# Performance work log

Hardware: AMD Instinct MI355X
Metric: run time of the kernel (lower is better)

## Reference

```python
import jax, jax.numpy as jnp
import numpy as np

D = 64        # inner_feature_len (dim)
HID = 128     # hidden_channels of the edge MLP
NCONV = 2     # n_conv
STEPS = 3     # Set2Set processing_steps
NSEG = 128    # number of graphs in the batch


def setup_inputs() -> dict:
    key = jax.random.key(0)
    ks = jax.random.split(key, 30)
    N, E, FN, FE = 10000, 64000, 92, 41
    s = 0.05
    p = lambda i, shape: jax.random.normal(ks[i], shape, jnp.float32) * s
    return {
        "x": jax.random.normal(ks[0], (N, FN), jnp.float32),
        "edge_attr": jax.random.uniform(ks[1], (E, FE), dtype=jnp.float32),
        "lin0_w": p(2, (D, FN)), "lin0_b": p(3, (D,)),
        "nn1_w": p(4, (HID, FE)), "nn1_b": p(5, (HID,)),
        "nn2_w": p(6, (D * D, HID)), "nn2_b": p(7, (D * D,)),
        "root_w": p(8, (D, D)), "conv_b": p(9, (D,)),
        "gru_w_ih": p(10, (3 * D, D)), "gru_w_hh": p(11, (3 * D, D)),
        "gru_b_ih": p(12, (3 * D,)), "gru_b_hh": p(13, (3 * D,)),
        "lstm_w_ih": p(14, (4 * D, 2 * D)), "lstm_w_hh": p(15, (4 * D, D)),
        "lstm_b_ih": p(16, (4 * D,)), "lstm_b_hh": p(17, (4 * D,)),
        "lin1_w": p(18, (D, 2 * D)), "lin1_b": p(19, (D,)),
        "lin2_w": p(20, (1, D)), "lin2_b": p(21, (1,)),
        "edge_index": jax.random.randint(ks[22], (2, E), 0, N, dtype=jnp.int32),
        "batch": jnp.sort(jax.random.randint(ks[23], (N,), 0, NSEG, dtype=jnp.int32)),
    }


def _gru_step(m, h, w_ih, w_hh, b_ih, b_hh):
    # torch GRU gate order: r, z, n
    gi = m @ w_ih.T + b_ih
    gh = h @ w_hh.T + b_hh
    r = jax.nn.sigmoid(gi[:, :D] + gh[:, :D])
    z = jax.nn.sigmoid(gi[:, D:2 * D] + gh[:, D:2 * D])
    n = jnp.tanh(gi[:, 2 * D:] + r * gh[:, 2 * D:])
    return (1.0 - z) * n + z * h


def _forward(x, edge_attr, lin0_w, lin0_b, nn1_w, nn1_b, nn2_w, nn2_b, root_w, conv_b,
             gru_w_ih, gru_w_hh, gru_b_ih, gru_b_hh, lstm_w_ih, lstm_w_hh, lstm_b_ih,
             lstm_b_hh, lin1_w, lin1_b, lin2_w, lin2_b, edge_index, batch):
    N = x.shape[0]
    src, dst = edge_index[0], edge_index[1]

    # Edge-conditioned weight matrices: [E, D, D] (dominant intermediate)
    We = (jax.nn.relu(edge_attr @ nn1_w.T + nn1_b) @ nn2_w.T + nn2_b).reshape(-1, D, D)
    deg = jnp.clip(jax.ops.segment_sum(jnp.ones_like(src, jnp.float32), dst, num_segments=N), 1.0, None)

    out = jax.nn.relu(x @ lin0_w.T + lin0_b)   # [N, D]
    h = out                                     # GRU hidden (num_layers=1)
    for _ in range(NCONV):
        # NNConv: gather -> per-edge matmul -> scatter-mean, plus root transform + bias
        msg = jnp.einsum('ei,eio->eo', out[src], We)                 # [E, D]
        agg = jax.ops.segment_sum(msg, dst, num_segments=N) / deg[:, None]
        m = jax.nn.relu(agg + out @ root_w.T + conv_b)
        h = _gru_step(m, h, gru_w_ih, gru_w_hh, gru_b_ih, gru_b_hh)
        out = h

    # Set2Set pooling (LSTM-attention readout)
    q_star = jnp.zeros((NSEG, 2 * D), x.dtype)
    hl = jnp.zeros((NSEG, D), x.dtype)
    cl = jnp.zeros((NSEG, D), x.dtype)
    for _ in range(STEPS):
        g = q_star @ lstm_w_ih.T + lstm_b_ih + hl @ lstm_w_hh.T + lstm_b_hh
        i = jax.nn.sigmoid(g[:, :D])
        f = jax.nn.sigmoid(g[:, D:2 * D])
        gg = jnp.tanh(g[:, 2 * D:3 * D])
        o = jax.nn.sigmoid(g[:, 3 * D:])
        cl = f * cl + i * gg
        hl = o * jnp.tanh(cl)
        q = hl                                   # [NSEG, D]
        e = jnp.sum(out * q[batch], axis=-1)     # [N]
        mmax = jax.ops.segment_max(e, batch, num_segments=NSEG)
        a = jnp.exp(e - mmax[batch])
        denom = jax.ops.segment_sum(a, batch, num_segments=NSEG)
        a = a / denom[batch]
        r = jax.ops.segment_sum(a[:, None] * out, batch, num_segments=NSEG)  # [NSEG, D]
        q_star = jnp.concatenate([q, r], axis=1)

    y = jax.nn.relu(q_star @ lin1_w.T + lin1_b) @ lin2_w.T + lin2_b
    return y.reshape(-1)


def reference(x, edge_attr, lin0_w, lin0_b, nn1_w, nn1_b, nn2_w, nn2_b, root_w, conv_b,
              gru_w_ih, gru_w_hh, gru_b_ih, gru_b_hh, lstm_w_ih, lstm_w_hh, lstm_b_ih,
              lstm_b_hh, lin1_w, lin1_b, lin2_w, lin2_b, edge_index, batch):
    return _forward(x, edge_attr, lin0_w, lin0_b, nn1_w, nn1_b, nn2_w, nn2_b, root_w,
                    conv_b, gru_w_ih, gru_w_hh, gru_b_ih, gru_b_hh, lstm_w_ih, lstm_w_hh,
                    lstm_b_ih, lstm_b_hh, lin1_w, lin1_b, lin2_w, lin2_b, edge_index, batch)
```

## Files before the change

### kernel.cpp

```cpp
#include <hip/hip_runtime.h>
#include <hip/hip_bf16.h>
#include <math.h>

#define DD 64
#define HIDC 128
#define FN 92
#define FE 41
#define S2CAP 192

typedef unsigned short u16;
typedef short bf16x8 __attribute__((ext_vector_type(8)));
typedef float f32x4 __attribute__((ext_vector_type(4)));
typedef u16 u16x8 __attribute__((ext_vector_type(8)));

__device__ __forceinline__ float sigmoidf_(float x){ return 1.f/(1.f+expf(-x)); }

__device__ __forceinline__ u16 f2bf(float v){
  union { float f; unsigned u; } x; x.f = v;
  unsigned r = x.u + 0x7fff + ((x.u >> 16) & 1);
  return (u16)(r >> 16);
}
__device__ __forceinline__ float bf2f(u16 v){
  union { float f; unsigned u; } x; x.u = ((unsigned)v) << 16;
  return x.f;
}
__device__ __forceinline__ void split_bf(float v, u16& h, u16& l){
  h = f2bf(v); l = f2bf(v - bf2f(h));
}

__global__ void k_pack(const float* __restrict__ lin0_w, const float* __restrict__ nn1_w,
                       const float* __restrict__ root_w, const float* __restrict__ gwih,
                       const float* __restrict__ gwhh, const float* __restrict__ lwih,
                       const float* __restrict__ lwhh, const float* __restrict__ lin1_w,
                       float* __restrict__ lin0T, float* __restrict__ nn1T,
                       float* __restrict__ rootT, float* __restrict__ wihT,
                       float* __restrict__ whhT, float* __restrict__ lwihT,
                       float* __restrict__ lwhhT, float* __restrict__ lin1T)
{
  int idx = blockIdx.x*blockDim.x + threadIdx.x;
  if (idx < 92*64){ int k=idx/64, o=idx%64; lin0T[k*64+o] = lin0_w[o*92+k]; return; } idx -= 92*64;
  if (idx < 41*128){ int k=idx/128, h=idx%128; nn1T[k*128+h] = nn1_w[h*41+k]; return; } idx -= 41*128;
  if (idx < 64*64){ int i=idx/64, o=idx%64; rootT[i*64+o] = root_w[o*64+i]; return; } idx -= 64*64;
  if (idx < 64*192){ int i=idx/192, g=idx%192; wihT[i*192+g] = gwih[g*64+i]; return; } idx -= 64*192;
  if (idx < 64*192){ int i=idx/192, g=idx%192; whhT[i*192+g] = gwhh[g*64+i]; return; } idx -= 64*192;
  if (idx < 128*256){ int j=idx/256, t=idx%256; lwihT[j*256+t] = lwih[t*128+j]; return; } idx -= 128*256;
  if (idx < 64*256){ int j=idx/256, t=idx%256; lwhhT[j*256+t] = lwhh[t*64+j]; return; } idx -= 64*256;
  if (idx < 128*64){ int j=idx/64, t=idx%64; lin1T[j*64+t] = lin1_w[t*128+j]; return; }
}

__global__ void k_pack_b2(const float* __restrict__ nn2_w,
                          u16* __restrict__ BhT, u16* __restrict__ BlT){
  int idx = blockIdx.x*256 + threadIdx.x;
  if (idx >= 524288) return;
  int i  = idx & 63;
  int ho = (idx >> 6) & 4095;
  int c  = idx >> 18;
  int h = ho >> 6, o = ho & 63;
  float v = nn2_w[(size_t)(i*64+o)*128 + c*64 + h];
  u16 hi, lo; split_bf(v, hi, lo);
  BhT[idx] = hi; BlT[idx] = lo;
}

__global__ void k_pack_b1(const float* __restrict__ nn1_w,
                          u16* __restrict__ BT1h, u16* __restrict__ BT1l){
  int idx = blockIdx.x*256 + threadIdx.x;
  if (idx >= 8192) return;
  int h = idx >> 6, k = idx & 63;
  float v = (k < FE) ? nn1_w[(size_t)h*FE + k] : 0.f;
  u16 hi, lo; split_bf(v, hi, lo);
  BT1h[idx] = hi; BT1l[idx] = lo;
}

__global__ void k_split_ea(const float* __restrict__ ea, const int* __restrict__ sortedE,
                           u16* __restrict__ eaH, u16* __restrict__ eaL, int E){
  int idx = blockIdx.x*256 + threadIdx.x;
  if (idx >= E*64) return;
  int ew = idx >> 6, k = idx & 63;
  int e = sortedE[ew];
  float v = (k < FE) ? ea[(size_t)e*FE + k] : 0.f;
  u16 hi, lo; split_bf(v, hi, lo);
  eaH[idx] = hi; eaL[idx] = lo;
}

__global__ __launch_bounds__(256) void k_node_mlp(const float* __restrict__ x,
    const float* __restrict__ lin0T, const float* __restrict__ lin0_b,
    const float* __restrict__ nn2_b,
    float* __restrict__ out, u16* __restrict__ outH, u16* __restrict__ outL,
    float* __restrict__ bterm, int N)
{
  __shared__ float xs[16][FN];
  const int w = threadIdx.x>>6, o = threadIdx.x&63;
  const int nb = blockIdx.x*16 + w*4;
  for (int idx = o; idx < 4*FN; idx += 64){
    int j = idx/FN, k = idx%FN;
    int n = nb + j;
    xs[w*4+j][k] = (n<N) ? x[(size_t)n*FN + k] : 0.f;
  }
  float acc[4];
  float bv = lin0_b[o];
  #pragma unroll
  for (int j=0;j<4;j++) acc[j] = bv;
  for (int k=0;k<FN;k++){
    float lw = lin0T[k*64+o];
    #pragma unroll
    for (int j=0;j<4;j++) acc[j] = fmaf(xs[w*4+j][k], lw, acc[j]);
  }
  float v[4];
  #pragma unroll
  for (int j=0;j<4;j++){
    v[j] = fmaxf(acc[j], 0.f);
    int n = nb + j;
    if (n < N){
      out[(size_t)n*64+o] = v[j];
      u16 hi, lo; split_bf(v[j], hi, lo);
      outH[(size_t)n*64+o] = hi;
      outL[(size_t)n*64+o] = lo;
    }
  }
  float bt[4] = {0.f,0.f,0.f,0.f};
  for (int i=0;i<64;i++){
    float wnb = nn2_b[i*64+o];
    #pragma unroll
    for (int j=0;j<4;j++) bt[j] = fmaf(__shfl(v[j], i, 64), wnb, bt[j]);
  }
  #pragma unroll
  for (int j=0;j<4;j++){
    int n = nb + j;
    if (n < N) bterm[(size_t)n*64+o] = bt[j];
  }
}

__global__ void k_count(const int* __restrict__ dst, const int* __restrict__ src,
                        float* __restrict__ deg, int* __restrict__ scnt, int E){
  int e = blockIdx.x*blockDim.x + threadIdx.x;
  if (e < E){
    atomicAdd(&deg[dst[e]], 1.f);
    atomicAdd(&scnt[src[e]], 1);
  }
}

__global__ void k_scan1(const int* __restrict__ cnt, int* __restrict__ excl,
                        int* __restrict__ bsum, int N){
  __shared__ int buf[256];
  int i = blockIdx.x*256 + threadIdx.x;
  int v = (i<N) ? cnt[i] : 0;
  buf[threadIdx.x] = v;
  __syncthreads();
  #pragma unroll
  for (int off=1; off<256; off<<=1){
    int t = (threadIdx.x>=off) ? buf[threadIdx.x-off] : 0;
    __syncthreads();
    buf[threadIdx.x] += t;
    __syncthreads();
  }
  if (i<N) excl[i] = buf[threadIdx.x] - v;
  if (threadIdx.x==255) bsum[blockIdx.x] = buf[255];
}
__global__ void k_scan2(int* __restrict__ bsum, int nb){
  __shared__ int buf[256];
  int v = (threadIdx.x<nb) ? bsum[threadIdx.x] : 0;
  buf[threadIdx.x] = v;
  __syncthreads();
  #pragma unroll
  for (int off=1; off<256; off<<=1){
    int t = (threadIdx.x>=off) ? buf[threadIdx.x-off] : 0;
    __syncthreads();
    buf[threadIdx.x] += t;
    __syncthreads();
  }
  if (threadIdx.x<nb) bsum[threadIdx.x] = buf[threadIdx.x] - v;
}
__global__ void k_scan3(int* __restrict__ starts, int* __restrict__ cursor,
                        const int* __restrict__ bsum, int N, int E){
  int i = blockIdx.x*256 + threadIdx.x;
  if (i<N){
    int s = starts[i] + bsum[blockIdx.x];
    starts[i] = s;
    cursor[i] = s;
  }
  if (i==0) starts[N] = E;
}

__global__ void k_sort(const int* __restrict__ src, const int* __restrict__ dst,
                       int* __restrict__ cursor, int* __restrict__ sortedE,
                       int* __restrict__ dstS, int E){
  int e = blockIdx.x*256 + threadIdx.x;
  if (e < E){
    int s = src[e];
    int p = atomicAdd(&cursor[s], 1);
    sortedE[p] = e;
    dstS[p] = dst[e];
  }
}

__global__ __launch_bounds__(256,3) void k_edge_mlp_mfma(
    const u16* __restrict__ eaH, const u16* __restrict__ eaL,
    const u16* __restrict__ BT1h, const u16* __restrict__ BT1l,
    const float* __restrict__ nn1_b, float* __restrict__ hidden, int E)
{
  const int lane = threadIdx.x & 63;
  const int wave = threadIdx.x >> 6;
  const int row  = lane & 15;
  const int quad = lane >> 4;
  const int m0 = blockIdx.x*128 + (wave>>1)*64;
  const int n0 = (wave&1)*64;

  bf16x8 AH0[4], AH1[4], AL0[4], AL1[4];
  #pragma unroll
  for (int p=0;p<4;p++){
    int ar = min(m0 + p*16 + row, E-1);
    const u16* aH = eaH + (size_t)ar*64 + quad*8;
    const u16* aL = eaL + (size_t)ar*64 + quad*8;
    AH0[p] = *(const bf16x8*)(aH);
    AH1[p] = *(const bf16x8*)(aH + 32);
    AL0[p] = *(const bf16x8*)(aL);
    AL1[p] = *(const bf16x8*)(aL + 32);
  }
  #pragma unroll
  for (int tb=0;tb<4;tb++){
    const u16* bH = BT1h + (size_t)(n0 + tb*16 + row)*64 + quad*8;
    const u16* bL = BT1l + (size_t)(n0 + tb*16 + row)*64 + quad*8;
    bf16x8 bh0 = *(const bf16x8*)(bH);
    bf16x8 bh1 = *(const bf16x8*)(bH + 32);
    bf16x8 bl0 = *(const bf16x8*)(bL);
    bf16x8 bl1 = *(const bf16x8*)(bL + 32);
    float4 bias;
    {
      int nb = n0 + tb*16 + quad*4;
      bias.x = nn1_b[nb+0]; bias.y = nn1_b[nb+1];
      bias.z = nn1_b[nb+2]; bias.w = nn1_b[nb+3];
    }
    #pragma unroll
    for (int ta=0;ta<4;ta++){
      f32x4 a = {0.f,0.f,0.f,0.f};
      a = __builtin_amdgcn_mfma_f32_16x16x32_bf16(bh0, AH0[ta], a, 0,0,0);
      a = __builtin_amdgcn_mfma_f32_16x16x32_bf16(bh1, AH1[ta], a, 0,0,0);
      a = __builtin_amdgcn_mfma_f32_16x16x32_bf16(bl0, AH0[ta], a, 0,0,0);
      a = __builtin_amdgcn_mfma_f32_16x16x32_bf16(bl1, AH1[ta], a, 0,0,0);
      a = __builtin_amdgcn_mfma_f32_16x16x32_bf16(bh0, AL0[ta], a, 0,0,0);
      a = __builtin_amdgcn_mfma_f32_16x16x32_bf16(bh1, AL1[ta], a, 0,0,0);
      int m = m0 + ta*16 + row;
      if (m < E){
        float4 v;
        v.x = fmaxf(a[0]+bias.x, 0.f); v.y = fmaxf(a[1]+bias.y, 0.f);
        v.z = fmaxf(a[2]+bias.z, 0.f); v.w = fmaxf(a[3]+bias.w, 0.f);
        *(float4*)(hidden + (size_t)m*128 + n0 + tb*16 + quad*4) = v;
      }
    }
  }
}

__global__ __launch_bounds__(256,3) void k_qgemm_mfma(
    const u16* __restrict__ Ah, const u16* __restrict__ Al,
    const u16* __restrict__ BhT, const u16* __restrict__ BlT,
    u16* __restrict__ C, int M, int QS, int cbase)
{
  const int lane = threadIdx.x & 63;
  const int wave = threadIdx.x >> 6;
  const int row  = lane & 15;
  const int quad = lane >> 4;
  const int m0 = blockIdx.y * 64;
  const int col = cbase + blockIdx.x * 256 + wave * 64;
  const int chunk = col >> 12;
  const int n0 = col & 4095;
  const u16* Bh = BhT + (size_t)chunk*262144;
  const u16* Bl = BlT + (size_t)chunk*262144;

  bf16x8 AH0[4], AH1[4], AL0[4], AL1[4];
  #pragma unroll
  for (int p=0;p<4;p++){
    int ar = min(m0 + p*16 + row, M-1);
    const u16* aH = Ah + (size_t)ar*64 + quad*8;
    const u16* aL = Al + (size_t)ar*64 + quad*8;
    AH0[p] = *(const bf16x8*)(aH);
    AH1[p] = *(const bf16x8*)(aH + 32);
    AL0[p] = *(const bf16x8*)(aL);
    AL1[p] = *(const bf16x8*)(aL + 32);
  }

  f32x4 acc[4][4];
  #pragma unroll
  for (int ta=0;ta<4;ta++)
    #pragma unroll
    for (int tb=0;tb<4;tb++)
      acc[ta][tb] = (f32x4){0.f,0.f,0.f,0.f};

  #pragma unroll
  for (int tb=0;tb<4;tb++){
    const u16* bH = Bh + (size_t)(n0 + tb*16 + row)*64 + quad*8;
    const u16* bL = Bl + (size_t)(n0 + tb*16 + row)*64 + quad*8;
    bf16x8 bh0 = *(const bf16x8*)(bH);
    bf16x8 bh1 = *(const bf16x8*)(bH + 32);
    bf16x8 bl0 = *(const bf16x8*)(bL);
    bf16x8 bl1 = *(const bf16x8*)(bL + 32);
    #pragma unroll
    for (int ta=0;ta<4;ta++){
      f32x4 a = acc[ta][tb];
      a = __builtin_amdgcn_mfma_f32_16x16x32_bf16(bh0, AH0[ta], a, 0,0,0);
      a = __builtin_amdgcn_mfma_f32_16x16x32_bf16(bh1, AH1[ta], a, 0,0,0);
      a = __builtin_amdgcn_mfma_f32_16x16x32_bf16(bl0, AH0[ta], a, 0,0,0);
      a = __builtin_amdgcn_mfma_f32_16x16x32_bf16(bl1, AH1[ta], a, 0,0,0);
      a = __builtin_amdgcn_mfma_f32_16x16x32_bf16(bh0, AL0[ta], a, 0,0,0);
      a = __builtin_amdgcn_mfma_f32_16x16x32_bf16(bh1, AL1[ta], a, 0,0,0);
      acc[ta][tb] = a;
    }
  }

  #pragma unroll
  for (int ta=0;ta<4;ta++){
    int m = m0 + ta*16 + row;
    if (m >= M) continue;
    u16* dst = C + (size_t)m*QS + (col - cbase) + quad*8;
    #pragma unroll
    for (int p=0;p<2;p++){
      f32x4 aa = acc[ta][2*p];
      f32x4 ab = acc[ta][2*p+1];
      u16x8 v;
      v[0]=f2bf(aa[0]); v[1]=f2bf(aa[1]); v[2]=f2bf(aa[2]); v[3]=f2bf(aa[3]);
      v[4]=f2bf(ab[0]); v[5]=f2bf(ab[1]); v[6]=f2bf(ab[2]); v[7]=f2bf(ab[3]);
      *(u16x8*)(dst + p*32) = v;
    }
  }
}

template<int NH>
__global__ __launch_bounds__(256) void k_edge_gather(const u16* __restrict__ Q,
    const float* __restrict__ hidden, int h0, int addbt,
    const float* __restrict__ bterm, const int* __restrict__ starts,
    const int* __restrict__ dstS, float* __restrict__ agg, int N)
{
  constexpr int NJ = NH/4;
  constexpr int QS = NH*64;
  __shared__ float red[4][64];
  const int wv = threadIdx.x>>6, lane = threadIdx.x&63;
  const int n = blockIdx.x*4 + wv;
  if (n >= N) return;
  const int e0 = starts[n], e1 = starts[n+1];
  if (e0 >= e1) return;
  const int sg = lane>>4, oq = lane&15;
  const int posb = ((oq>>3)<<5) + ((oq&3)<<3) + (((oq>>2)&1)<<2);
  const u16* qp = Q + (size_t)n*QS + sg*64 + posb;
  ushort4 qreg[NJ];
  #pragma unroll
  for (int j=0;j<NJ;j++) qreg[j] = *(const ushort4*)(qp + (size_t)j*256);
  const float bt = addbt ? bterm[(size_t)n*64 + lane] : 0.f;

  float hA = hidden[(size_t)e0*128 + h0 + lane];
  float hB = (NH==128) ? hidden[(size_t)e0*128 + h0 + 64 + lane] : 0.f;
  int dN = dstS[e0];
  for (int e=e0; e<e1; ++e){
    const float h0v = hA, h1v = hB;
    const int d = dN;
    if (e+1 < e1){
      hA = hidden[(size_t)(e+1)*128 + h0 + lane];
      if (NH==128) hB = hidden[(size_t)(e+1)*128 + h0 + 64 + lane];
      dN = dstS[e+1];
    }
    float a0=0.f,a1=0.f,a2=0.f,a3=0.f;
    #pragma unroll
    for (int j=0;j<NJ;j++){
      float h4 = __shfl((j<16) ? h0v : h1v, ((j*4)&63)+sg, 64);
      a0 = fmaf(h4, bf2f(qreg[j].x), a0);
      a1 = fmaf(h4, bf2f(qreg[j].y), a1);
      a2 = fmaf(h4, bf2f(qreg[j].z), a2);
      a3 = fmaf(h4, bf2f(qreg[j].w), a3);
    }
    a0 += __shfl_xor(a0,16); a0 += __shfl_xor(a0,32);
    a1 += __shfl_xor(a1,16); a1 += __shfl_xor(a1,32);
    a2 += __shfl_xor(a2,16); a2 += __shfl_xor(a2,32);
    a3 += __shfl_xor(a3,16); a3 += __shfl_xor(a3,32);
    if (lane < 16){
      float4 r; r.x=a0; r.y=a1; r.z=a2; r.w=a3;
      *(float4*)&red[wv][lane*4] = r;
    }
    atomicAdd(&agg[(size_t)d*64 + lane], bt + red[wv][lane]);
  }
}

__global__ __launch_bounds__(256) void k_node_update(const float* __restrict__ outOld,
    const float* __restrict__ agg, const float* __restrict__ deg,
    const float* __restrict__ rootT, const float* __restrict__ conv_b,
    const float* __restrict__ wihT, const float* __restrict__ whhT,
    const float* __restrict__ b_ih, const float* __restrict__ b_hh,
    const float* __restrict__ nn2_b,
    float* __restrict__ outNew, u16* __restrict__ outH, u16* __restrict__ outL,
    float* __restrict__ bterm, int N)
{
  __shared__ float hs[16][64];
  __shared__ float ms[16][64];
  const int w = threadIdx.x>>6, o = threadIdx.x&63;
  const int nb = blockIdx.x*16 + w*4;
  float h[4];
  #pragma unroll
  for (int j=0;j<4;j++){
    int n = nb+j;
    h[j] = (n<N) ? outOld[(size_t)n*64+o] : 0.f;
    hs[w*4+j][o] = h[j];
  }
  float root[4] = {0.f,0.f,0.f,0.f};
  for (int i=0;i<64;i++){
    float rw = rootT[i*64+o];
    #pragma unroll
    for (int j=0;j<4;j++) root[j] = fmaf(hs[w*4+j][i], rw, root[j]);
  }
  float cb = conv_b[o];
  float m[4];
  #pragma unroll
  for (int j=0;j<4;j++){
    int n = nb+j;
    float d = (n<N) ? fmaxf(deg[n], 1.f) : 1.f;
    float a = (n<N) ? agg[(size_t)n*64+o]/d : 0.f;
    m[j] = fmaxf(a + root[j] + cb, 0.f);
    ms[w*4+j][o] = m[j];
  }
  float gir[4],giz[4],gin[4],ghr[4],ghz[4],ghn[4];
  float bir=b_ih[o], biz=b_ih[64+o], bin=b_ih[128+o];
  float bhr=b_hh[o], bhz=b_hh[64+o], bhn=b_hh[128+o];
  #pragma unroll
  for (int j=0;j<4;j++){
    gir[j]=bir; giz[j]=biz; gin[j]=bin;
    ghr[j]=bhr; ghz[j]=bhz; ghn[j]=bhn;
  }
  for (int i=0;i<64;i++){
    float wr=wihT[i*192+o], wz=wihT[i*192+64+o], wn=wihT[i*192+128+o];
    float vr=whhT[i*192+o], vz=whhT[i*192+64+o], vn=whhT[i*192+128+o];
    #pragma unroll
    for (int j=0;j<4;j++){
      float mi = ms[w*4+j][i], hi = hs[w*4+j][i];
      gir[j]=fmaf(mi,wr,gir[j]); giz[j]=fmaf(mi,wz,giz[j]); gin[j]=fmaf(mi,wn,gin[j]);
      ghr[j]=fmaf(hi,vr,ghr[j]); ghz[j]=fmaf(hi,vz,ghz[j]); ghn[j]=fmaf(hi,vn,ghn[j]);
    }
  }
  float v[4];
  #pragma unroll
  for (int j=0;j<4;j++){
    float r = sigmoidf_(gir[j]+ghr[j]);
    float z = sigmoidf_(giz[j]+ghz[j]);
    float nn = tanhf(gin[j] + r*ghn[j]);
    v[j] = (1.f-z)*nn + z*h[j];
    int n = nb+j;
    if (n<N){
      outNew[(size_t)n*64+o] = v[j];
      u16 hi16, lo16; split_bf(v[j], hi16, lo16);
      outH[(size_t)n*64+o] = hi16;
      outL[(size_t)n*64+o] = lo16;
    }
  }
  float bt[4] = {0.f,0.f,0.f,0.f};
  for (int i=0;i<64;i++){
    float wnb = nn2_b[i*64+o];
    #pragma unroll
    for (int j=0;j<4;j++) bt[j] = fmaf(__shfl(v[j], i, 64), wnb, bt[j]);
  }
  #pragma unroll
  for (int j=0;j<4;j++){
    int n = nb+j;
    if (n<N) bterm[(size_t)n*64+o] = bt[j];
  }
}

__global__ __launch_bounds__(256) void k_set2set(const float* __restrict__ out,
    const int* __restrict__ batch, int N,
    const float* __restrict__ lwihT, const float* __restrict__ lwhhT,
    const float* __restrict__ b_ih, const float* __restrict__ b_hh,
    const float* __restrict__ lin1T, const float* __restrict__ lin1_b,
    const float* __restrict__ lin2_w, const float* __restrict__ lin2_b,
    float* __restrict__ y)
{
  __shared__ float X[S2CAP][65];
  __shared__ float earr[S2CAP];
  __shared__ float qstar[128], hl[64], cl[64], g[256];
  __shared__ float rpart[4][64], spart[4], redm[4], zs[64];
  __shared__ int sb[2];
  const int tid = threadIdx.x;
  const int b = blockIdx.x;
  const int wid = tid>>6, lane = tid&63;
  if (tid < 128) qstar[tid] = 0.f;
  if (tid < 64){ hl[tid]=0.f; cl[tid]=0.f; }
  if (tid == 0){
    int lo=0, hi=N;
    while (lo<hi){ int mid=(lo+hi)>>1; if (batch[mid] < b) lo=mid+1; else hi=mid; }
    sb[0]=lo;
    int lo2=lo, hi2=N;
    while (lo2<hi2){ int mid=(lo2+hi2)>>1; if (batch[mid] < b+1) lo2=mid+1; else hi2=mid; }
    sb[1]=lo2;
  }
  __syncthreads();
  const int nlo = sb[0], nhi = sb[1], nn = nhi - nlo;
  const bool single = (nn <= S2CAP);
  if (single){
    for (int idx = tid; idx < nn*64; idx += 256){
      X[idx>>6][idx&63] = out[(size_t)(nlo + (idx>>6))*64 + (idx&63)];
    }
  }
  __syncthreads();

  for (int step=0; step<3; step++){
    float gs = b_ih[tid] + b_hh[tid];
    for (int j=0;j<128;j++) gs = fmaf(qstar[j], lwihT[j*256+tid], gs);
    for (int j=0;j<64;j++)  gs = fmaf(hl[j],    lwhhT[j*256+tid], gs);
    g[tid] = gs;
    __syncthreads();
    if (tid < 64){
      float ig = sigmoidf_(g[tid]);
      float fg = sigmoidf_(g[64+tid]);
      float gg = tanhf(g[128+tid]);
      float og = sigmoidf_(g[192+tid]);
      float c = fg*cl[tid] + ig*gg;
      cl[tid] = c;
      hl[tid] = og*tanhf(c);
    }
    __syncthreads();

    if (single){
      float lm = -INFINITY;
      for (int n = tid; n < nn; n += 256){
        float acc = 0.f;
        #pragma unroll 8
        for (int d=0; d<64; d++) acc = fmaf(X[n][d], hl[d], acc);
        earr[n] = acc;
        lm = fmaxf(lm, acc);
      }
      lm = fmaxf(lm, __shfl_xor(lm,1));  lm = fmaxf(lm, __shfl_xor(lm,2));
      lm = fmaxf(lm, __shfl_xor(lm,4));  lm = fmaxf(lm, __shfl_xor(lm,8));
      lm = fmaxf(lm, __shfl_xor(lm,16)); lm = fmaxf(lm, __shfl_xor(lm,32));
      if (lane==0) redm[wid] = lm;
      __syncthreads();
      if (tid==0) redm[0] = fmaxf(fmaxf(redm[0],redm[1]), fmaxf(redm[2],redm[3]));
      __syncthreads();
      const float gmax = redm[0];
      float ls = 0.f;
      for (int n = tid; n < nn; n += 256){
        float a = expf(earr[n] - gmax);
        earr[n] = a;
        ls += a;
      }
      ls += __shfl_xor(ls,1);  ls += __shfl_xor(ls,2);  ls += __shfl_xor(ls,4);
      ls += __shfl_xor(ls,8);  ls += __shfl_xor(ls,16); ls += __shfl_xor(ls,32);
      if (lane==0) spart[wid] = ls;
      __syncthreads();
      float racc = 0.f;
      for (int n = wid; n < nn; n += 4) racc = fmaf(earr[n], X[n][lane], racc);
      rpart[wid][lane] = racc;
      __syncthreads();
      if (tid < 64){
        float r = rpart[0][tid]+rpart[1][tid]+rpart[2][tid]+rpart[3][tid];
        float s = spart[0]+spart[1]+spart[2]+spart[3];
        qstar[tid] = hl[tid];
        qstar[64+tid] = (nn>0) ? r/s : 0.f;
      }
      __syncthreads();
    } else {
      float qv = hl[lane];
      float lm = -INFINITY;
      for (int n = nlo + wid; n < nhi; n += 4){
        float p = out[(size_t)n*64 + lane]*qv;
        p += __shfl_xor(p,1); p += __shfl_xor(p,2); p += __shfl_xor(p,4);
        p += __shfl_xor(p,8); p += __shfl_xor(p,16); p += __shfl_xor(p,32);
        lm = fmaxf(lm, p);
      }
      if (lane==0) redm[wid] = lm;
      __syncthreads();
      if (tid==0) redm[0] = fmaxf(fmaxf(redm[0],redm[1]), fmaxf(redm[2],redm[3]));
      __syncthreads();
      float gmax = redm[0];
      float sw = 0.f, racc = 0.f;
      for (int n = nlo + wid; n < nhi; n += 4){
        float ol = out[(size_t)n*64 + lane];
        float p = ol*qv;
        p += __shfl_xor(p,1); p += __shfl_xor(p,2); p += __shfl_xor(p,4);
        p += __shfl_xor(p,8); p += __shfl_xor(p,16); p += __shfl_xor(p,32);
        float a = expf(p - gmax);
        sw += a;
        racc = fmaf(a, ol, racc);
      }
      rpart[wid][lane] = racc;
      if (lane==0) spart[wid] = sw;
      __syncthreads();
      if (tid < 64){
        float r = rpart[0][tid]+rpart[1][tid]+rpart[2][tid]+rpart[3][tid];
        float s = spart[0]+spart[1]+spart[2]+spart[3];
        qstar[tid] = hl[tid];
        qstar[64+tid] = (nn>0) ? r/s : 0.f;
      }
      __syncthreads();
    }
  }
  if (tid < 64){
    float acc = lin1_b[tid];
    for (int j=0;j<128;j++) acc = fmaf(qstar[j], lin1T[j*64+tid], acc);
    zs[tid] = fmaxf(acc, 0.f);
  }
  __syncthreads();
  if (tid < 64){
    float v = zs[lane]*lin2_w[lane];
    v += __shfl_xor(v,1); v += __shfl_xor(v,2); v += __shfl_xor(v,4);
    v += __shfl_xor(v,8); v += __shfl_xor(v,16); v += __shfl_xor(v,32);
    if (lane==0) y[b] = v + lin2_b[0];
  }
}

extern "C" void kernel_launch(void* const* d_in, const int* in_sizes, int n_in,
                              void* d_out, int out_size, void* d_ws, size_t ws_size,
                              hipStream_t stream)
{
  const float* x      = (const float*)d_in[0];
  const float* eattr  = (const float*)d_in[1];
  const float* lin0_w = (const float*)d_in[2];
  const float* lin0_b = (const float*)d_in[3];
  const float* nn1_w  = (const float*)d_in[4];
  const float* nn1_b  = (const float*)d_in[5];
  const float* nn2_w  = (const float*)d_in[6];
  const float* nn2_b  = (const float*)d_in[7];
  const float* root_w = (const float*)d_in[8];
  const float* conv_b = (const float*)d_in[9];
  const float* gwih   = (const float*)d_in[10];
  const float* gwhh   = (const float*)d_in[11];
  const float* gbih   = (const float*)d_in[12];
  const float* gbhh   = (const float*)d_in[13];
  const float* lwih   = (const float*)d_in[14];
  const float* lwhh   = (const float*)d_in[15];
  const float* lbih   = (const float*)d_in[16];
  const float* lbhh   = (const float*)d_in[17];
  const float* lin1_w = (const float*)d_in[18];
  const float* lin1_b = (const float*)d_in[19];
  const float* lin2_w = (const float*)d_in[20];
  const float* lin2_b = (const float*)d_in[21];
  const int*   eidx   = (const int*)d_in[22];
  const int*   batch  = (const int*)d_in[23];

  const int N = in_sizes[0]/FN;
  const int E = in_sizes[1]/FE;
  const int* srcI = eidx;
  const int* dstI = eidx + E;

  char* w = (char*)d_ws;
  size_t off = 0;
  auto alloc = [&](size_t bytes)->char* {
    char* p = w + off;
    off = (off + bytes + 255) & ~(size_t)255;
    return p;
  };
  float* degw  = (float*)alloc((size_t)N*4);
  int*   scnt  = (int*)alloc((size_t)N*4);
  int*   starts= (int*)alloc((size_t)(N+1)*4);
  int*   cursor= (int*)alloc((size_t)N*4);
  int*   bsum  = (int*)alloc((size_t)256*4);
  int*   sortedE=(int*)alloc((size_t)E*4);
  int*   dstS  = (int*)alloc((size_t)E*4);
  float* outA  = (float*)alloc((size_t)N*64*4);
  float* outB  = (float*)alloc((size_t)N*64*4);
  u16*   outAH = (u16*)alloc((size_t)N*64*2);
  u16*   outAL = (u16*)alloc((size_t)N*64*2);
  u16*   outBH = (u16*)alloc((size_t)N*64*2);
  u16*   outBL = (u16*)alloc((size_t)N*64*2);
  float* agg   = (float*)alloc((size_t)N*64*4);
  float* bterm = (float*)alloc((size_t)N*64*4);
  float* hidden= (float*)alloc((size_t)E*128*4);
  u16*   B2hT  = (u16*)alloc((size_t)524288*2);
  u16*   B2lT  = (u16*)alloc((size_t)524288*2);
  u16*   BT1h  = (u16*)alloc((size_t)8192*2);
  u16*   BT1l  = (u16*)alloc((size_t)8192*2);
  float* lin0T = (float*)alloc((size_t)92*64*4);
  float* nn1T  = (float*)alloc((size_t)41*128*4);
  float* rootT = (float*)alloc((size_t)64*64*4);
  float* wihT  = (float*)alloc((size_t)64*192*4);
  float* whhT  = (float*)alloc((size_t)64*192*4);
  float* lwihT = (float*)alloc((size_t)128*256*4);
  float* lwhhT = (float*)alloc((size_t)64*256*4);
  float* lin1T = (float*)alloc((size_t)128*64*4);

  size_t qbig = (size_t)N*8192*2;
  size_t qsmall = (size_t)N*4096*2;
  bool merged = (ws_size - off) >= (qbig + 512);
  u16* Q = (u16*)alloc(merged ? qbig : qsmall);
  u16* eaH = (u16*)Q;
  u16* eaL = eaH + (size_t)E*64;

  const int NB = (N+255)/256;

  hipMemsetAsync(degw, 0, (size_t)N*4, stream);
  hipMemsetAsync(scnt, 0, (size_t)N*4, stream);
  k_pack<<<(97152+255)/256, 256, 0, stream>>>(lin0_w, nn1_w, root_w, gwih, gwhh,
      lwih, lwhh, lin1_w, lin0T, nn1T, rootT, wihT, whhT, lwihT, lwhhT, lin1T);
  k_pack_b2<<<524288/256, 256, 0, stream>>>(nn2_w, B2hT, B2lT);
  k_pack_b1<<<8192/256, 256, 0, stream>>>(nn1_w, BT1h, BT1l);
  k_node_mlp<<<(N+15)/16, 256, 0, stream>>>(x, lin0T, lin0_b, nn2_b, outA, outAH, outAL, bterm, N);
  k_count<<<(E+255)/256, 256, 0, stream>>>(dstI, srcI, degw, scnt, E);
  k_scan1<<<NB, 256, 0, stream>>>(scnt, starts, bsum, N);
  k_scan2<<<1, 256, 0, stream>>>(bsum, NB);
  k_scan3<<<NB, 256, 0, stream>>>(starts, cursor, bsum, N, E);
  k_sort<<<(E+255)/256, 256, 0, stream>>>(srcI, dstI, cursor, sortedE, dstS, E);
  k_split_ea<<<((size_t)E*64+255)/256, 256, 0, stream>>>(eattr, sortedE, eaH, eaL, E);
  k_edge_mlp_mfma<<<(E+127)/128, 256, 0, stream>>>(eaH, eaL, BT1h, BT1l, nn1_b, hidden, E);

  float* cur = outA; float* nxt = outB;
  u16* curH = outAH; u16* curL = outAL;
  u16* nxtH = outBH; u16* nxtL = outBL;
  const int gatherG = (N+3)/4;
  for (int conv=0; conv<2; conv++){
    hipMemsetAsync(agg, 0, (size_t)N*64*4, stream);
    if (merged){
      k_qgemm_mfma<<<dim3(32,(N+63)/64), 256, 0, stream>>>(curH, curL, B2hT, B2lT, Q, N, 8192, 0);
      k_edge_gather<128><<<gatherG, 256, 0, stream>>>(Q, hidden, 0, 1, bterm, starts, dstS, agg, N);
    } else {
      for (int c=0; c<2; c++){
        k_qgemm_mfma<<<dim3(16,(N+63)/64), 256, 0, stream>>>(curH, curL, B2hT, B2lT, Q, N, 4096, c*4096);
        k_edge_gather<64><<<gatherG, 256, 0, stream>>>(Q, hidden, c*64, (c==0)?1:0, bterm, starts, dstS, agg, N);
      }
    }
    k_node_update<<<(N+15)/16, 256, 0, stream>>>(cur, agg, degw, rootT, conv_b,
        wihT, whhT, gbih, gbhh, nn2_b, nxt, nxtH, nxtL, bterm, N);
    float* t = cur; cur = nxt; nxt = t;
    u16* th = curH; curH = nxtH; nxtH = th;
    u16* tl = curL; curL = nxtL; nxtL = tl;
  }

  k_set2set<<<128, 256, 0, stream>>>(cur, batch, N, lwihT, lwhhT, lbih, lbhh,
      lin1T, lin1_b, lin2_w, lin2_b, (float*)d_out);
}
```

Measured before the change: 601.9 us.

## Store Q in column-block-major layout and split edge gather into two passes

```diff
diff --git a/kernel.cpp b/kernel.cpp
--- a/kernel.cpp
+++ b/kernel.cpp
@@ -253,7 +253,7 @@
 __global__ __launch_bounds__(256,3) void k_qgemm_mfma(
     const u16* __restrict__ Ah, const u16* __restrict__ Al,
     const u16* __restrict__ BhT, const u16* __restrict__ BlT,
-    u16* __restrict__ C, int M, int QS, int cbase)
+    u16* __restrict__ C, int M, int cbase)
 {
   const int lane = threadIdx.x & 63;
   const int wave = threadIdx.x >> 6;
@@ -306,11 +306,12 @@
     }
   }
 
+  const int cbl = (col - cbase) >> 6;
   #pragma unroll
   for (int ta=0;ta<4;ta++){
     int m = m0 + ta*16 + row;
     if (m >= M) continue;
-    u16* dst = C + (size_t)m*QS + (col - cbase) + quad*8;
+    u16* dst = C + ((size_t)cbl*M + m)*64 + quad*8;
     #pragma unroll
     for (int p=0;p<2;p++){
       f32x4 aa = acc[ta][2*p];
@@ -323,14 +324,12 @@
   }
 }
 
-template<int NH>
 __global__ __launch_bounds__(256) void k_edge_gather(const u16* __restrict__ Q,
-    const float* __restrict__ hidden, int h0, int addbt,
+    const float* __restrict__ hidden, int h0, int cb0, int addbt,
     const float* __restrict__ bterm, const int* __restrict__ starts,
     const int* __restrict__ dstS, float* __restrict__ agg, int N)
 {
-  constexpr int NJ = NH/4;
-  constexpr int QS = NH*64;
+  __shared__ float hs[4][64];
   __shared__ float red[4][64];
   const int wv = threadIdx.x>>6, lane = threadIdx.x&63;
   const int n = blockIdx.x*4 + wv;
@@ -339,27 +338,27 @@
   if (e0 >= e1) return;
   const int sg = lane>>4, oq = lane&15;
   const int posb = ((oq>>3)<<5) + ((oq&3)<<3) + (((oq>>2)&1)<<2);
-  const u16* qp = Q + (size_t)n*QS + sg*64 + posb;
-  ushort4 qreg[NJ];
-  #pragma unroll
-  for (int j=0;j<NJ;j++) qreg[j] = *(const ushort4*)(qp + (size_t)j*256);
+  const u16* qp = Q + ((size_t)(cb0+sg)*N + n)*64 + posb;
+  const size_t jstride = (size_t)N*256;
+  ushort4 qreg[16];
+  #pragma unroll
+  for (int j=0;j<16;j++) qreg[j] = *(const ushort4*)(qp + (size_t)j*jstride);
   const float bt = addbt ? bterm[(size_t)n*64 + lane] : 0.f;
 
-  float hA = hidden[(size_t)e0*128 + h0 + lane];
-  float hB = (NH==128) ? hidden[(size_t)e0*128 + h0 + 64 + lane] : 0.f;
-  int dN = dstS[e0];
+  float hvN = hidden[(size_t)e0*128 + h0 + lane];
+  int   dN  = dstS[e0];
   for (int e=e0; e<e1; ++e){
-    const float h0v = hA, h1v = hB;
-    const int d = dN;
+    const float hv = hvN;
+    const int   d  = dN;
     if (e+1 < e1){
-      hA = hidden[(size_t)(e+1)*128 + h0 + lane];
-      if (NH==128) hB = hidden[(size_t)(e+1)*128 + h0 + 64 + lane];
-      dN = dstS[e+1];
-    }
+      hvN = hidden[(size_t)(e+1)*128 + h0 + lane];
+      dN  = dstS[e+1];
+    }
+    hs[wv][lane] = hv;
     float a0=0.f,a1=0.f,a2=0.f,a3=0.f;
     #pragma unroll
-    for (int j=0;j<NJ;j++){
-      float h4 = __shfl((j<16) ? h0v : h1v, ((j*4)&63)+sg, 64);
+    for (int j=0;j<16;j++){
+      float h4 = hs[wv][j*4+sg];
       a0 = fmaf(h4, bf2f(qreg[j].x), a0);
       a1 = fmaf(h4, bf2f(qreg[j].y), a1);
       a2 = fmaf(h4, bf2f(qreg[j].z), a2);
@@ -701,12 +700,13 @@
   for (int conv=0; conv<2; conv++){
     hipMemsetAsync(agg, 0, (size_t)N*64*4, stream);
     if (merged){
-      k_qgemm_mfma<<<dim3(32,(N+63)/64), 256, 0, stream>>>(curH, curL, B2hT, B2lT, Q, N, 8192, 0);
-      k_edge_gather<128><<<gatherG, 256, 0, stream>>>(Q, hidden, 0, 1, bterm, starts, dstS, agg, N);
+      k_qgemm_mfma<<<dim3(32,(N+63)/64), 256, 0, stream>>>(curH, curL, B2hT, B2lT, Q, N, 0);
+      k_edge_gather<<<gatherG, 256, 0, stream>>>(Q, hidden, 0,  0,  1, bterm, starts, dstS, agg, N);
+      k_edge_gather<<<gatherG, 256, 0, stream>>>(Q, hidden, 64, 64, 0, bterm, starts, dstS, agg, N);
     } else {
       for (int c=0; c<2; c++){
-        k_qgemm_mfma<<<dim3(16,(N+63)/64), 256, 0, stream>>>(curH, curL, B2hT, B2lT, Q, N, 4096, c*4096);
-        k_edge_gather<64><<<gatherG, 256, 0, stream>>>(Q, hidden, c*64, (c==0)?1:0, bterm, starts, dstS, agg, N);
+        k_qgemm_mfma<<<dim3(16,(N+63)/64), 256, 0, stream>>>(curH, curL, B2hT, B2lT, Q, N, c*4096);
+        k_edge_gather<<<gatherG, 256, 0, stream>>>(Q, hidden, c*64, 0, (c==0)?1:0, bterm, starts, dstS, agg, N);
       }
     }
     k_node_update<<<(N+15)/16, 256, 0, stream>>>(cur, agg, degw, rootT, conv_b,
```

Result: faster. 587.6 us (-2.4%).

## Tile Q into 64x64 slabs and broadcast hidden values via LDS in gather

Applied to the files above, without the earlier changes.

```diff
diff --git a/kernel.cpp b/kernel.cpp
--- a/kernel.cpp
+++ b/kernel.cpp
@@ -253,7 +253,7 @@
 __global__ __launch_bounds__(256,3) void k_qgemm_mfma(
     const u16* __restrict__ Ah, const u16* __restrict__ Al,
     const u16* __restrict__ BhT, const u16* __restrict__ BlT,
-    u16* __restrict__ C, int M, int QS, int cbase)
+    u16* __restrict__ C, int M, int cbase, int nslab)
 {
   const int lane = threadIdx.x & 63;
   const int wave = threadIdx.x >> 6;
@@ -306,11 +306,13 @@
     }
   }
 
+  const int cbl = (col - cbase) >> 6;
+  u16* base = C + (((size_t)blockIdx.y*nslab + cbl)*64)*64;
   #pragma unroll
   for (int ta=0;ta<4;ta++){
     int m = m0 + ta*16 + row;
     if (m >= M) continue;
-    u16* dst = C + (size_t)m*QS + (col - cbase) + quad*8;
+    u16* dst = base + (size_t)(m & 63)*64 + quad*8;
     #pragma unroll
     for (int p=0;p<2;p++){
       f32x4 aa = acc[ta][2*p];
@@ -330,7 +332,9 @@
     const int* __restrict__ dstS, float* __restrict__ agg, int N)
 {
   constexpr int NJ = NH/4;
-  constexpr int QS = NH*64;
+  constexpr int NHALF = NH/64;
+  constexpr int NSLAB = NH;
+  __shared__ float hs[4][NHALF][64];
   __shared__ float red[4][64];
   const int wv = threadIdx.x>>6, lane = threadIdx.x&63;
   const int n = blockIdx.x*4 + wv;
@@ -339,27 +343,29 @@
   if (e0 >= e1) return;
   const int sg = lane>>4, oq = lane&15;
   const int posb = ((oq>>3)<<5) + ((oq&3)<<3) + (((oq>>2)&1)<<2);
-  const u16* qp = Q + (size_t)n*QS + sg*64 + posb;
+  const u16* qp = Q + (((size_t)(n>>6)*NSLAB + sg)*64 + (n&63))*64 + posb;
   ushort4 qreg[NJ];
   #pragma unroll
-  for (int j=0;j<NJ;j++) qreg[j] = *(const ushort4*)(qp + (size_t)j*256);
+  for (int j=0;j<NJ;j++) qreg[j] = *(const ushort4*)(qp + (size_t)j*16384);
   const float bt = addbt ? bterm[(size_t)n*64 + lane] : 0.f;
 
-  float hA = hidden[(size_t)e0*128 + h0 + lane];
-  float hB = (NH==128) ? hidden[(size_t)e0*128 + h0 + 64 + lane] : 0.f;
-  int dN = dstS[e0];
+  float hvA = hidden[(size_t)e0*128 + h0 + lane];
+  float hvB = (NHALF==2) ? hidden[(size_t)e0*128 + h0 + 64 + lane] : 0.f;
+  int   dN  = dstS[e0];
   for (int e=e0; e<e1; ++e){
-    const float h0v = hA, h1v = hB;
-    const int d = dN;
+    const float h0v = hvA, h1v = hvB;
+    const int   d  = dN;
     if (e+1 < e1){
-      hA = hidden[(size_t)(e+1)*128 + h0 + lane];
-      if (NH==128) hB = hidden[(size_t)(e+1)*128 + h0 + 64 + lane];
-      dN = dstS[e+1];
-    }
+      hvA = hidden[(size_t)(e+1)*128 + h0 + lane];
+      if (NHALF==2) hvB = hidden[(size_t)(e+1)*128 + h0 + 64 + lane];
+      dN  = dstS[e+1];
+    }
+    hs[wv][0][lane] = h0v;
+    if (NHALF==2) hs[wv][1][lane] = h1v;
     float a0=0.f,a1=0.f,a2=0.f,a3=0.f;
     #pragma unroll
     for (int j=0;j<NJ;j++){
-      float h4 = __shfl((j<16) ? h0v : h1v, ((j*4)&63)+sg, 64);
+      float h4 = hs[wv][j>>4][((j*4)&63)+sg];
       a0 = fmaf(h4, bf2f(qreg[j].x), a0);
       a1 = fmaf(h4, bf2f(qreg[j].y), a1);
       a2 = fmaf(h4, bf2f(qreg[j].z), a2);
@@ -670,8 +676,9 @@
   float* lwhhT = (float*)alloc((size_t)64*256*4);
   float* lin1T = (float*)alloc((size_t)128*64*4);
 
-  size_t qbig = (size_t)N*8192*2;
-  size_t qsmall = (size_t)N*4096*2;
+  const int Npad = ((N+63)/64)*64;
+  size_t qbig = (size_t)Npad*8192*2;
+  size_t qsmall = (size_t)Npad*4096*2;
   bool merged = (ws_size - off) >= (qbig + 512);
   u16* Q = (u16*)alloc(merged ? qbig : qsmall);
   u16* eaH = (u16*)Q;
@@ -701,11 +708,11 @@
   for (int conv=0; conv<2; conv++){
     hipMemsetAsync(agg, 0, (size_t)N*64*4, stream);
     if (merged){
-      k_qgemm_mfma<<<dim3(32,(N+63)/64), 256, 0, stream>>>(curH, curL, B2hT, B2lT, Q, N, 8192, 0);
+      k_qgemm_mfma<<<dim3(32,(N+63)/64), 256, 0, stream>>>(curH, curL, B2hT, B2lT, Q, N, 0, 128);
       k_edge_gather<128><<<gatherG, 256, 0, stream>>>(Q, hidden, 0, 1, bterm, starts, dstS, agg, N);
     } else {
       for (int c=0; c<2; c++){
-        k_qgemm_mfma<<<dim3(16,(N+63)/64), 256, 0, stream>>>(curH, curL, B2hT, B2lT, Q, N, 4096, c*4096);
+        k_qgemm_mfma<<<dim3(16,(N+63)/64), 256, 0, stream>>>(curH, curL, B2hT, B2lT, Q, N, c*4096, 64);
         k_edge_gather<64><<<gatherG, 256, 0, stream>>>(Q, hidden, c*64, (c==0)?1:0, bterm, starts, dstS, agg, N);
       }
     }
```

Result: faster. 586.1 us (-2.6%).
